# Performance work log

Measured on AMD Instinct MI355X. Metric: run time of the kernel, lower is better.

Reference implementation:

```python
import jax, jax.numpy as jnp
import numpy as np

N, E = 100000, 1600000
ENT, OCU, SAI, IJ = 64, 64, 64, 8


def setup_inputs() -> dict:
    key = jax.random.key(0)
    ks = jax.random.split(key, 14)

    def lin(k, fan_in, fan_out):
        s = 1.0 / np.sqrt(fan_in)
        kw, kb = jax.random.split(k)
        w = jax.random.uniform(kw, (fan_in, fan_out), minval=-s, maxval=s, dtype=jnp.float32)
        b = jax.random.uniform(kb, (fan_out,), minval=-s, maxval=s, dtype=jnp.float32)
        return w, b

    we_w1, we_b1 = lin(ks[0], 2 * ENT + 1 + IJ, OCU)
    we_w2, we_b2 = lin(ks[1], OCU, OCU)
    wx_w1, wx_b1 = lin(ks[2], OCU, OCU)
    wx_w2, wx_b2 = lin(ks[3], OCU, 1)
    wh_w1, wh_b1 = lin(ks[4], ENT + OCU, OCU)
    wh_w2, wh_b2 = lin(ks[5], OCU, SAI)
    wv_w1, wv_b1 = lin(ks[6], ENT, OCU)
    wv_w2, wv_b2 = lin(ks[7], OCU, 1)

    return {
        "h": jax.random.normal(ks[8], (N, ENT), dtype=jnp.float32),
        "x": jax.random.normal(ks[9], (N, 3), dtype=jnp.float32),
        "velocidade": jax.random.normal(ks[10], (N, 3), dtype=jnp.float32),
        "atributos_arestas": jax.random.normal(ks[11], (E, IJ), dtype=jnp.float32),
        "we_w1": we_w1, "we_b1": we_b1, "we_w2": we_w2, "we_b2": we_b2,
        "wx_w1": wx_w1, "wx_b1": wx_b1, "wx_w2": wx_w2, "wx_b2": wx_b2,
        "wh_w1": wh_w1, "wh_b1": wh_b1, "wh_w2": wh_w2, "wh_b2": wh_b2,
        "wv_w1": wv_w1, "wv_b1": wv_b1, "wv_w2": wv_w2, "wv_b2": wv_b2,
        "arestas": jax.random.randint(ks[12], (2, E), 0, N, dtype=jnp.int32),
    }


def reference(h, x, velocidade, atributos_arestas,
              we_w1, we_b1, we_w2, we_b2,
              wx_w1, wx_b1, wx_w2, wx_b2,
              wh_w1, wh_b1, wh_w2, wh_b2,
              wv_w1, wv_b1, wv_w2, wv_b2,
              arestas):
    linhas, cols = arestas[0], arestas[1]
    n = h.shape[0]

    # gather endpoint coordinates, radial distance per edge
    diferenca = x[linhas] - x[cols]                            # [E, 3]
    dif_radial = jnp.sum(diferenca * diferenca, axis=1, keepdims=True)  # [E, 1]

    # edge MLP phi_e on [h_i, h_j, ||x_i-x_j||^2, edge_attr]
    atributos = jnp.concatenate([h[linhas], h[cols], dif_radial, atributos_arestas], axis=1)
    m_ij = jnp.tanh(jnp.tanh(atributos @ we_w1 + we_b1) @ we_w2 + we_b2)   # [E, OCU]

    # phi_x: per-edge scalar gate on coordinate differences
    phi_x = jnp.tanh(jnp.tanh(m_ij @ wx_w1 + wx_b1) @ wx_w2 + wx_b2)       # [E, 1]

    # phi_v: per-node scalar gate on velocity
    phi_v = jnp.tanh(h @ wv_w1 + wv_b1) @ wv_w2 + wv_b2                    # [N, 1]

    # segment-mean of (diferenca * phi_x) over source nodes
    trans = diferenca * phi_x                                              # [E, 3]
    agg_sum = jax.ops.segment_sum(trans, linhas, num_segments=n)           # [N, 3]
    cnt = jax.ops.segment_sum(jnp.ones((E, 1), trans.dtype), linhas, num_segments=n)
    agg_mean = agg_sum / jnp.maximum(cnt, 1.0)

    velocidade_nova = velocidade * phi_v + agg_mean
    x_nova = x + velocidade_nova

    # segment-sum of edge messages, node update phi_h
    m_i = jax.ops.segment_sum(m_ij, linhas, num_segments=n)                # [N, OCU]
    h_cat = jnp.concatenate([h, m_i], axis=1)
    h_nova = jnp.tanh(h_cat @ wh_w1 + wh_b1) @ wh_w2 + wh_b2               # [N, SAI]

    return (h_nova, x_nova, velocidade_nova)
```

## Files before the change

### kernel.cpp

```cpp
#include <hip/hip_runtime.h>


typedef unsigned int uint;
typedef unsigned short u16;
typedef __attribute__((ext_vector_type(8))) short short8;
typedef __attribute__((ext_vector_type(4))) float f32x4;

#define UB_LO(u) __uint_as_float((u) << 16)
#define UB_HI(u) __uint_as_float((u) & 0xffff0000u)

__device__ __forceinline__ float fast_tanh(float x) {
    float e = __expf(2.0f * x);
    return 1.0f - 2.0f * __builtin_amdgcn_rcpf(e + 1.0f);
}
__device__ __forceinline__ u16 bf16rne(float f) {
    uint u = __float_as_uint(f);
    return (u16)((u + 0x7fffu + ((u >> 16) & 1u)) >> 16);
}
__device__ __forceinline__ uint packbf(float a, float b) {
    return (uint)bf16rne(a) | ((uint)bf16rne(b) << 16);
}
__device__ __forceinline__ uint packbf_fast(float a, float b) {
    return __builtin_amdgcn_perm(__float_as_uint(b), __float_as_uint(a), 0x07060302u);
}
__device__ __forceinline__ u16 trunc16(float f) {
    return (u16)(__float_as_uint(f) >> 16);
}
__device__ __forceinline__ int swzb(int b) { return b ^ ((b >> 3) & 0x70); }

__global__ void wprep_kernel(const float* __restrict__ we_w1, const float* __restrict__ we_w2,
                             const float* __restrict__ wx_w1, const float* __restrict__ wv_w1,
                             const float* __restrict__ wh_w1, const float* __restrict__ wh_w2,
                             u16* __restrict__ we1t, u16* __restrict__ we2t,
                             u16* __restrict__ wx1t, u16* __restrict__ wv1t,
                             u16* __restrict__ wh1t, u16* __restrict__ wh2t,
                             u16* __restrict__ wert) {
    int t = blockIdx.x * 256 + threadIdx.x;
    if (t < 8192) {
        int j = t >> 7, k = t & 127;
        we1t[t] = bf16rne(we_w1[k * 64 + j]);
        wh1t[t] = bf16rne(wh_w1[k * 64 + j]);
    }
    if (t < 4096) {
        int n = t >> 6, k = t & 63;
        we2t[t] = bf16rne(we_w2[k * 64 + n]);
        wx1t[t] = bf16rne(wx_w1[k * 64 + n]);
        wv1t[t] = bf16rne(wv_w1[k * 64 + n]);
        wh2t[t] = bf16rne(wh_w2[k * 64 + n]);
    }
    if (t < 2048) {
        int n = t >> 5, k = t & 31;
        float v = 0.0f;
        if (k == 0) v = we_w1[128 * 64 + n];
        else if (k <= 8) v = we_w1[(128 + k) * 64 + n];
        wert[t] = bf16rne(v);
    }
}

__global__ __launch_bounds__(256, 2)
void pre_mfma_kernel(const float* __restrict__ h, const float* __restrict__ we_b1,
                     const u16* __restrict__ we1t,
                     u16* __restrict__ HrB, u16* __restrict__ HcB, int N)
{
    __shared__ u16 X1[4096];
    __shared__ u16 X2[4096];
    const int tid = threadIdx.x, lane = tid & 63, wv = tid >> 6;
    const int nb = blockIdx.x * 64;
    const int el = tid >> 2, jg = tid & 3;
    const int fn = lane & 15, fk8 = (lane >> 4) * 8;

    {
        uint pk[8];
        if (nb + el < N) {
            const float4* h4 = (const float4*)(h + (size_t)(nb + el) * 64 + jg * 16);
            #pragma unroll
            for (int q = 0; q < 4; q++) {
                float4 v = h4[q];
                pk[2*q]   = packbf_fast(v.x, v.y);
                pk[2*q+1] = packbf_fast(v.z, v.w);
            }
        } else {
            #pragma unroll
            for (int q = 0; q < 8; q++) pk[q] = 0;
        }
        const int b0 = swzb(el * 128 + jg * 32), b1 = swzb(el * 128 + jg * 32 + 16);
        *(uint4*)(&X1[b0 >> 1]) = make_uint4(pk[0], pk[1], pk[2], pk[3]);
        *(uint4*)(&X1[b1 >> 1]) = make_uint4(pk[4], pk[5], pk[6], pk[7]);
    }
    __syncthreads();

    const int mb = wv * 16;
    short8 a0, a1;
    {
        const int ba = swzb((mb + fn) * 128 + fk8 * 2);
        const int bb = swzb((mb + fn) * 128 + 64 + fk8 * 2);
        a0 = *(const short8*)(&X1[ba >> 1]);
        a1 = *(const short8*)(&X1[bb >> 1]);
    }
    #pragma unroll
    for (int n0 = 0; n0 < 4; n0++) {
        uint4 bw0 = *(const uint4*)(we1t + (n0*16 + fn) * 128 + fk8);
        uint4 bw1 = *(const uint4*)(we1t + (n0*16 + fn) * 128 + 32 + fk8);
        const float bias = we_b1[n0 * 16 + fn];
        f32x4 q = {bias, bias, bias, bias};
        q = __builtin_amdgcn_mfma_f32_16x16x32_bf16(a0, __builtin_bit_cast(short8, bw0), q, 0, 0, 0);
        q = __builtin_amdgcn_mfma_f32_16x16x32_bf16(a1, __builtin_bit_cast(short8, bw1), q, 0, 0, 0);
        #pragma unroll
        for (int r2 = 0; r2 < 4; r2++) {
            const int m = mb + (lane >> 4) * 4 + r2;
            X2[swzb(m * 128 + (n0*16 + fn) * 2) >> 1] = bf16rne(q[r2]);
        }
    }
    __syncthreads();
    if (nb + el < N) {
        const int b0 = swzb(el * 128 + jg * 32), b1 = swzb(el * 128 + jg * 32 + 16);
        uint4 v0 = *(const uint4*)(&X2[b0 >> 1]);
        uint4 v1 = *(const uint4*)(&X2[b1 >> 1]);
        u16* o = HrB + (size_t)(nb + el) * 64 + jg * 16;
        *(uint4*)o = v0; *(uint4*)(o + 8) = v1;
    }
    __syncthreads();
    #pragma unroll
    for (int n0 = 0; n0 < 4; n0++) {
        uint4 bw0 = *(const uint4*)(we1t + (n0*16 + fn) * 128 + 64 + fk8);
        uint4 bw1 = *(const uint4*)(we1t + (n0*16 + fn) * 128 + 96 + fk8);
        f32x4 q = {0.f, 0.f, 0.f, 0.f};
        q = __builtin_amdgcn_mfma_f32_16x16x32_bf16(a0, __builtin_bit_cast(short8, bw0), q, 0, 0, 0);
        q = __builtin_amdgcn_mfma_f32_16x16x32_bf16(a1, __builtin_bit_cast(short8, bw1), q, 0, 0, 0);
        #pragma unroll
        for (int r2 = 0; r2 < 4; r2++) {
            const int m = mb + (lane >> 4) * 4 + r2;
            X2[swzb(m * 128 + (n0*16 + fn) * 2) >> 1] = bf16rne(q[r2]);
        }
    }
    __syncthreads();
    if (nb + el < N) {
        const int b0 = swzb(el * 128 + jg * 32), b1 = swzb(el * 128 + jg * 32 + 16);
        uint4 v0 = *(const uint4*)(&X2[b0 >> 1]);
        uint4 v1 = *(const uint4*)(&X2[b1 >> 1]);
        u16* o = HcB + (size_t)(nb + el) * 64 + jg * 16;
        *(uint4*)o = v0; *(uint4*)(o + 8) = v1;
    }
}

__global__ __launch_bounds__(256, 8)
void edge_mfma_kernel(const float* __restrict__ x, const float* __restrict__ eattr,
                      const int* __restrict__ perm, const int2* __restrict__ rc,
                      const u16* __restrict__ HrB, const u16* __restrict__ HcB,
                      const u16* __restrict__ wert,
                      const u16* __restrict__ we2t, const float* __restrict__ we_b2,
                      const u16* __restrict__ wx1t, const float* __restrict__ wx_b1,
                      const float* __restrict__ wx_w2, const float* __restrict__ wx_b2,
                      float* __restrict__ miF, float* __restrict__ aggF,
                      float* __restrict__ cntF, int E)
{
    __shared__ u16 T[4096];
    __shared__ float dS[64][3];
    __shared__ float pxS[64];
    __shared__ float radS[64];
    __shared__ int rS[64];

    const int tid = threadIdx.x, lane = tid & 63, wv = tid >> 6;
    int bid = blockIdx.x;
    const int nwg = gridDim.x;
    if ((nwg & 7) == 0) bid = (bid & 7) * (nwg >> 3) + (bid >> 3);
    const int sb = bid * 64;
    const int fn = lane & 15, fk8 = (lane >> 4) * 8;
    const int el = tid >> 2, jg = tid & 3;
    const int s = sb + el;
    const int mb = wv * 16;

    {
        int r = -1, c = 0;
        if (s < E) { int2 p2 = rc[s]; r = p2.x; c = p2.y; }
        if (jg == 0) rS[el] = r;
        uint pk[8];
        if (s < E) {
            if (jg == 0) {
                const float d0 = x[(size_t)r*3+0] - x[(size_t)c*3+0];
                const float d1 = x[(size_t)r*3+1] - x[(size_t)c*3+1];
                const float d2 = x[(size_t)r*3+2] - x[(size_t)c*3+2];
                dS[el][0] = d0; dS[el][1] = d1; dS[el][2] = d2;
                radS[el] = d0*d0 + d1*d1 + d2*d2;
            }
            uint4 ra = *(const uint4*)(HrB + (size_t)r * 64 + jg * 16);
            uint4 rb = *(const uint4*)(HrB + (size_t)r * 64 + jg * 16 + 8);
            uint4 ca = *(const uint4*)(HcB + (size_t)c * 64 + jg * 16);
            uint4 cb = *(const uint4*)(HcB + (size_t)c * 64 + jg * 16 + 8);
            uint rw[8] = {ra.x, ra.y, ra.z, ra.w, rb.x, rb.y, rb.z, rb.w};
            uint cw[8] = {ca.x, ca.y, ca.z, ca.w, cb.x, cb.y, cb.z, cb.w};
            #pragma unroll
            for (int q = 0; q < 8; q++) {
                const float lo = UB_LO(rw[q]) + UB_LO(cw[q]);
                const float hi = UB_HI(rw[q]) + UB_HI(cw[q]);
                pk[q] = packbf_fast(lo, hi);
            }
        } else {
            #pragma unroll
            for (int q = 0; q < 8; q++) pk[q] = 0;
        }
        const int b0 = swzb(el * 128 + jg * 32), b1 = swzb(el * 128 + jg * 32 + 16);
        *(uint4*)(&T[b0 >> 1]) = make_uint4(pk[0], pk[1], pk[2], pk[3]);
        *(uint4*)(&T[b1 >> 1]) = make_uint4(pk[4], pk[5], pk[6], pk[7]);
    }
    __syncthreads();

    uint ae[4] = {0, 0, 0, 0};
    {
        const int kc = lane >> 4;
        const int s2 = sb + mb + fn;
        if (kc < 2 && s2 < E) {
            const int e2 = perm[s2];
            const float4* ea4 = (const float4*)(eattr + (size_t)e2 * 8);
            if (kc == 0) {
                float4 u0 = ea4[0], u1 = ea4[1];
                const float rad = radS[mb + fn];
                ae[0] = packbf_fast(rad,  u0.x);
                ae[1] = packbf_fast(u0.y, u0.z);
                ae[2] = packbf_fast(u0.w, u1.x);
                ae[3] = packbf_fast(u1.y, u1.z);
            } else {
                float4 u1 = ea4[1];
                ae[0] = packbf_fast(u1.w, 0.0f);
            }
        }
    }
    const short8 a_e = __builtin_bit_cast(short8, *(uint4*)ae);

    #pragma unroll
    for (int n0 = 0; n0 < 4; n0++) {
        uint4 bw = *(const uint4*)(wert + (n0*16 + fn) * 32 + fk8);
        f32x4 q = {0.f, 0.f, 0.f, 0.f};
        q = __builtin_amdgcn_mfma_f32_16x16x32_bf16(a_e, __builtin_bit_cast(short8, bw), q, 0, 0, 0);
        #pragma unroll
        for (int r2 = 0; r2 < 4; r2++) {
            const int idx = swzb((mb + (lane >> 4) * 4 + r2) * 128 + (n0*16 + fn) * 2) >> 1;
            const float pre = q[r2] + UB_LO((uint)T[idx]);
            T[idx] = trunc16(fast_tanh(pre));
        }
    }

    short8 a0, a1;
    {
        const int ba = swzb((mb + fn) * 128 + fk8 * 2);
        const int bb = swzb((mb + fn) * 128 + 64 + fk8 * 2);
        a0 = *(const short8*)(&T[ba >> 1]);
        a1 = *(const short8*)(&T[bb >> 1]);
    }
    #pragma unroll
    for (int n0 = 0; n0 < 4; n0++) {
        uint4 bw0 = *(const uint4*)(we2t + (n0*16 + fn) * 64 + fk8);
        uint4 bw1 = *(const uint4*)(we2t + (n0*16 + fn) * 64 + 32 + fk8);
        const float bias = we_b2[n0 * 16 + fn];
        f32x4 q = {bias, bias, bias, bias};
        q = __builtin_amdgcn_mfma_f32_16x16x32_bf16(a0, __builtin_bit_cast(short8, bw0), q, 0, 0, 0);
        q = __builtin_amdgcn_mfma_f32_16x16x32_bf16(a1, __builtin_bit_cast(short8, bw1), q, 0, 0, 0);
        #pragma unroll
        for (int r2 = 0; r2 < 4; r2++) {
            const int m = mb + (lane >> 4) * 4 + r2;
            T[swzb(m * 128 + (n0*16 + fn) * 2) >> 1] = bf16rne(fast_tanh(q[r2]));
        }
    }

    short8 c0, c1;
    {
        const int ba = swzb((mb + fn) * 128 + fk8 * 2);
        const int bb = swzb((mb + fn) * 128 + 64 + fk8 * 2);
        c0 = *(const short8*)(&T[ba >> 1]);
        c1 = *(const short8*)(&T[bb >> 1]);
    }
    float pxp[4] = {0.f, 0.f, 0.f, 0.f};
    #pragma unroll
    for (int n0 = 0; n0 < 4; n0++) {
        uint4 bw0 = *(const uint4*)(wx1t + (n0*16 + fn) * 64 + fk8);
        uint4 bw1 = *(const uint4*)(wx1t + (n0*16 + fn) * 64 + 32 + fk8);
        const float bias = wx_b1[n0 * 16 + fn];
        f32x4 q = {bias, bias, bias, bias};
        q = __builtin_amdgcn_mfma_f32_16x16x32_bf16(c0, __builtin_bit_cast(short8, bw0), q, 0, 0, 0);
        q = __builtin_amdgcn_mfma_f32_16x16x32_bf16(c1, __builtin_bit_cast(short8, bw1), q, 0, 0, 0);
        const float wqn = wx_w2[n0 * 16 + fn];
        #pragma unroll
        for (int r2 = 0; r2 < 4; r2++) pxp[r2] += fast_tanh(q[r2]) * wqn;
    }
    #pragma unroll
    for (int off = 1; off < 16; off <<= 1) {
        #pragma unroll
        for (int r2 = 0; r2 < 4; r2++) pxp[r2] += __shfl_xor(pxp[r2], off, 64);
    }
    if (fn == 0) {
        const float bx2 = wx_b2[0];
        #pragma unroll
        for (int r2 = 0; r2 < 4; r2++) {
            const int m = mb + (lane >> 4) * 4 + r2;
            pxS[m] = fast_tanh(pxp[r2] + bx2);
        }
    }
    __syncthreads();

    const int w16 = wv * 16;
    for (int s0 = w16; s0 < w16 + 16; s0++) {
        const int r0 = rS[s0];
        if (r0 < 0) continue;
        if (s0 > 0 && rS[s0 - 1] == r0) continue;
        int s1 = s0 + 1;
        while (s1 < 64 && rS[s1] == r0) s1++;
        float msum = 0.0f, tsum = 0.0f;
        for (int t = s0; t < s1; t++) {
            msum += UB_LO((uint)T[swzb(t * 128 + lane * 2) >> 1]);
            if (lane < 3) tsum += dS[t][lane] * pxS[t];
        }
        atomicAdd(&miF[(size_t)r0 * 64 + lane], msum);
        if (lane < 3) atomicAdd(&aggF[(size_t)r0 * 3 + lane], tsum);
        if (lane == 3) atomicAdd(&cntF[r0], (float)(s1 - s0));
    }
}

__global__ __launch_bounds__(256, 2)
void aggnode_kernel(const float* __restrict__ h, const float* __restrict__ x,
                    const float* __restrict__ vel,
                    const float* __restrict__ miF, const float* __restrict__ aggF,
                    const float* __restrict__ cntF,
                    const u16* __restrict__ wv1t, const float* __restrict__ wv_b1,
                    const float* __restrict__ wv_w2, const float* __restrict__ wv_b2,
                    const u16* __restrict__ wh1t, const float* __restrict__ wh_b1,
                    const u16* __restrict__ wh2t, const float* __restrict__ wh_b2,
                    float* __restrict__ out_h, float* __restrict__ out_x,
                    float* __restrict__ out_v, int N)
{
    __shared__ u16 Xh[4096];
    __shared__ u16 Xm[4096];
    __shared__ float aggM[64][3];
    __shared__ float pvS[64];

    const int tid = threadIdx.x, lane = tid & 63, wv = tid >> 6;
    const int nb = blockIdx.x * 64;
    const int el = tid >> 2, jg = tid & 3;
    const int fn = lane & 15, fk8 = (lane >> 4) * 8;

    {
        uint pk[8];
        if (nb + el < N) {
            const float4* h4 = (const float4*)(h + (size_t)(nb + el) * 64 + jg * 16);
            #pragma unroll
            for (int q = 0; q < 4; q++) {
                float4 v = h4[q];
                pk[2*q]   = packbf_fast(v.x, v.y);
                pk[2*q+1] = packbf_fast(v.z, v.w);
            }
        } else {
            #pragma unroll
            for (int q = 0; q < 8; q++) pk[q] = 0;
        }
        const int b0 = swzb(el * 128 + jg * 32), b1 = swzb(el * 128 + jg * 32 + 16);
        *(uint4*)(&Xh[b0 >> 1]) = make_uint4(pk[0], pk[1], pk[2], pk[3]);
        *(uint4*)(&Xh[b1 >> 1]) = make_uint4(pk[4], pk[5], pk[6], pk[7]);
    }

    for (int t = 0; t < 16; t++) {
        const int ln = wv * 16 + t;
        const int n = nb + ln;
        float val = 0.0f;
        if (n < N) val = miF[(size_t)n * 64 + lane];
        Xm[swzb(ln * 128 + lane * 2) >> 1] = bf16rne(val);
        if (lane < 3 && n < N) {
            const float cf = cntF[n];
            aggM[ln][lane] = aggF[(size_t)n * 3 + lane] / fmaxf(cf, 1.0f);
        }
    }
    __syncthreads();

    const int mb = wv * 16;
    short8 a0, a1, b0, b1;
    {
        const int ba = swzb((mb + fn) * 128 + fk8 * 2);
        const int bb = swzb((mb + fn) * 128 + 64 + fk8 * 2);
        a0 = *(const short8*)(&Xh[ba >> 1]);
        a1 = *(const short8*)(&Xh[bb >> 1]);
        b0 = *(const short8*)(&Xm[ba >> 1]);
        b1 = *(const short8*)(&Xm[bb >> 1]);
    }

    float pvp[4] = {0.f, 0.f, 0.f, 0.f};
    #pragma unroll
    for (int n0 = 0; n0 < 4; n0++) {
        uint4 bw0 = *(const uint4*)(wv1t + (n0*16 + fn) * 64 + fk8);
        uint4 bw1 = *(const uint4*)(wv1t + (n0*16 + fn) * 64 + 32 + fk8);
        const float bias = wv_b1[n0 * 16 + fn];
        f32x4 q = {bias, bias, bias, bias};
        q = __builtin_amdgcn_mfma_f32_16x16x32_bf16(a0, __builtin_bit_cast(short8, bw0), q, 0, 0, 0);
        q = __builtin_amdgcn_mfma_f32_16x16x32_bf16(a1, __builtin_bit_cast(short8, bw1), q, 0, 0, 0);
        const float wqn = wv_w2[n0 * 16 + fn];
        #pragma unroll
        for (int r2 = 0; r2 < 4; r2++) pvp[r2] += fast_tanh(q[r2]) * wqn;
    }
    #pragma unroll
    for (int off = 1; off < 16; off <<= 1) {
        #pragma unroll
        for (int r2 = 0; r2 < 4; r2++) pvp[r2] += __shfl_xor(pvp[r2], off, 64);
    }
    if (fn == 0) {
        const float bv2 = wv_b2[0];
        #pragma unroll
        for (int r2 = 0; r2 < 4; r2++) pvS[mb + (lane >> 4) * 4 + r2] = pvp[r2] + bv2;
    }
    __syncthreads();

    #pragma unroll
    for (int n0 = 0; n0 < 4; n0++) {
        const u16* base = wh1t + (n0*16 + fn) * 128;
        uint4 bw0 = *(const uint4*)(base + fk8);
        uint4 bw1 = *(const uint4*)(base + 32 + fk8);
        uint4 bw2 = *(const uint4*)(base + 64 + fk8);
        uint4 bw3 = *(const uint4*)(base + 96 + fk8);
        const float bias = wh_b1[n0 * 16 + fn];
        f32x4 q = {bias, bias, bias, bias};
        q = __builtin_amdgcn_mfma_f32_16x16x32_bf16(a0, __builtin_bit_cast(short8, bw0), q, 0, 0, 0);
        q = __builtin_amdgcn_mfma_f32_16x16x32_bf16(a1, __builtin_bit_cast(short8, bw1), q, 0, 0, 0);
        q = __builtin_amdgcn_mfma_f32_16x16x32_bf16(b0, __builtin_bit_cast(short8, bw2), q, 0, 0, 0);
        q = __builtin_amdgcn_mfma_f32_16x16x32_bf16(b1, __builtin_bit_cast(short8, bw3), q, 0, 0, 0);
        #pragma unroll
        for (int r2 = 0; r2 < 4; r2++) {
            const int m = mb + (lane >> 4) * 4 + r2;
            Xm[swzb(m * 128 + (n0*16 + fn) * 2) >> 1] = bf16rne(fast_tanh(q[r2]));
        }
    }
    __syncthreads();

    short8 c0, c1;
    {
        const int ba = swzb((mb + fn) * 128 + fk8 * 2);
        const int bb = swzb((mb + fn) * 128 + 64 + fk8 * 2);
        c0 = *(const short8*)(&Xm[ba >> 1]);
        c1 = *(const short8*)(&Xm[bb >> 1]);
    }
    #pragma unroll
    for (int n0 = 0; n0 < 4; n0++) {
        uint4 bw0 = *(const uint4*)(wh2t + (n0*16 + fn) * 64 + fk8);
        uint4 bw1 = *(const uint4*)(wh2t + (n0*16 + fn) * 64 + 32 + fk8);
        const float bias = wh_b2[n0 * 16 + fn];
        f32x4 q = {bias, bias, bias, bias};
        q = __builtin_amdgcn_mfma_f32_16x16x32_bf16(c0, __builtin_bit_cast(short8, bw0), q, 0, 0, 0);
        q = __builtin_amdgcn_mfma_f32_16x16x32_bf16(c1, __builtin_bit_cast(short8, bw1), q, 0, 0, 0);
        #pragma unroll
        for (int r2 = 0; r2 < 4; r2++) {
            const int m = mb + (lane >> 4) * 4 + r2;
            if (nb + m < N) out_h[(size_t)(nb + m) * 64 + n0 * 16 + fn] = q[r2];
        }
    }

    if (tid < 64 && nb + tid < N) {
        const int n = nb + tid;
        const float pv = pvS[tid];
        #pragma unroll
        for (int d = 0; d < 3; d++) {
            const float am = aggM[tid][d];
            const float vn = vel[(size_t)n * 3 + d] * pv + am;
            out_v[(size_t)n * 3 + d] = vn;
            out_x[(size_t)n * 3 + d] = x[(size_t)n * 3 + d] + vn;
        }
    }
}

__global__ void hist_kernel(const int* __restrict__ rows, int* __restrict__ hist, int E) {
    int e = blockIdx.x * blockDim.x + threadIdx.x;
    if (e < E) atomicAdd(&hist[rows[e]], 1);
}

__global__ __launch_bounds__(256)
void scan1_kernel(const int* __restrict__ hist, int* __restrict__ bsum, int N) {
    const int t = threadIdx.x, b = blockIdx.x;
    const int base = b * 1024 + t * 4;
    int s = 0;
    #pragma unroll
    for (int q = 0; q < 4; q++) s += (base + q < N) ? hist[base + q] : 0;
    #pragma unroll
    for (int off = 1; off < 64; off <<= 1) s += __shfl_xor(s, off, 64);
    __shared__ int ws[4];
    if ((t & 63) == 0) ws[t >> 6] = s;
    __syncthreads();
    if (t == 0) bsum[b] = ws[0] + ws[1] + ws[2] + ws[3];
}

__global__ __launch_bounds__(256)
void scan2_kernel(int* __restrict__ bsum, int nb) {
    __shared__ int buf[1024];
    const int t = threadIdx.x;
    for (int i = t; i < nb; i += 256) buf[i] = bsum[i];
    __syncthreads();
    if (t == 0) {
        int run = 0;
        for (int i = 0; i < nb; i++) { int v = buf[i]; buf[i] = run; run += v; }
    }
    __syncthreads();
    for (int i = t; i < nb; i += 256) bsum[i] = buf[i];
}

__global__ __launch_bounds__(256)
void scan3_kernel(const int* __restrict__ hist, const int* __restrict__ bbase,
                  int* __restrict__ offs, int* __restrict__ cursor, int N) {
    const int t = threadIdx.x, b = blockIdx.x;
    const int base = b * 1024 + t * 4;
    int v[4];
    #pragma unroll
    for (int q = 0; q < 4; q++) v[q] = (base + q < N) ? hist[base + q] : 0;
    const int s = v[0] + v[1] + v[2] + v[3];
    const int lane = t & 63, wid = t >> 6;
    int inc = s;
    #pragma unroll
    for (int off = 1; off < 64; off <<= 1) {
        int u = __shfl_up(inc, off, 64);
        if (lane >= off) inc += u;
    }
    __shared__ int wtot[4];
    if (lane == 63) wtot[wid] = inc;
    __syncthreads();
    int wbase = 0;
    #pragma unroll
    for (int wq = 0; wq < 3; wq++) if (wq < wid) wbase += wtot[wq];
    int run = bbase[b] + wbase + (inc - s);
    #pragma unroll
    for (int q = 0; q < 4; q++) {
        const int i = base + q;
        if (i < N) { cursor[i] = run; run += v[q]; offs[i + 1] = run; }
    }
    if (b == 0 && t == 0) offs[0] = 0;
}

__global__ void scatter_kernel(const int* __restrict__ rows, const int* __restrict__ cols,
                               int* __restrict__ cursor,
                               int* __restrict__ perm, int2* __restrict__ rc, int E) {
    int e = blockIdx.x * blockDim.x + threadIdx.x;
    if (e < E) {
        int r = rows[e];
        int p = atomicAdd(&cursor[r], 1);
        perm[p] = e;
        rc[p] = make_int2(r, cols[e]);
    }
}

template<int BLK>
__global__ __launch_bounds__(BLK)
void edge_atomic_kernel(const float* __restrict__ h, const float* __restrict__ x,
                 const float* __restrict__ eattr,
                 const int* __restrict__ rows, const int* __restrict__ cols,
                 const float* __restrict__ we_w1, const float* __restrict__ we_b1,
                 const float* __restrict__ we_w2, const float* __restrict__ we_b2,
                 const float* __restrict__ wx_w1, const float* __restrict__ wx_b1,
                 const float* __restrict__ wx_w2, const float* __restrict__ wx_b2,
                 float* __restrict__ agg, float* __restrict__ cnt, float* __restrict__ mi,
                 int E)
{
    __shared__ float act[64][BLK];
    const int tid = threadIdx.x;
    const int e = blockIdx.x * BLK + tid;
    if (e >= E) return;

    const int r = rows[e];
    const int c = cols[e];
    const float d0 = x[(size_t)r*3+0] - x[(size_t)c*3+0];
    const float d1 = x[(size_t)r*3+1] - x[(size_t)c*3+1];
    const float d2 = x[(size_t)r*3+2] - x[(size_t)c*3+2];
    const float rad = d0*d0 + d1*d1 + d2*d2;

    float A[64];
    #pragma unroll
    for (int j = 0; j < 64; j++) A[j] = we_b1[j];
    const float* hr = h + (size_t)r * 64;
    const float* hc = h + (size_t)c * 64;
    #pragma unroll 4
    for (int k = 0; k < 64; k++) {
        const float a0 = hr[k];
        const float a1 = hc[k];
        const float* w0 = we_w1 + k * 64;
        const float* w1 = we_w1 + (64 + k) * 64;
        #pragma unroll
        for (int j = 0; j < 64; j++) A[j] += a0 * w0[j] + a1 * w1[j];
    }
    {
        const float* w = we_w1 + 128 * 64;
        #pragma unroll
        for (int j = 0; j < 64; j++) A[j] += rad * w[j];
    }
    const float* ea = eattr + (size_t)e * 8;
    #pragma unroll
    for (int k = 0; k < 8; k++) {
        const float a = ea[k];
        const float* w = we_w1 + (129 + k) * 64;
        #pragma unroll
        for (int j = 0; j < 64; j++) A[j] += a * w[j];
    }
    #pragma unroll
    for (int j = 0; j < 64; j++) act[j][tid] = fast_tanh(A[j]);

    float B[64];
    #pragma unroll
    for (int j = 0; j < 64; j++) B[j] = we_b2[j];
    #pragma unroll 4
    for (int k = 0; k < 64; k++) {
        const float a = act[k][tid];
        const float* w = we_w2 + k * 64;
        #pragma unroll
        for (int j = 0; j < 64; j++) B[j] += a * w[j];
    }
    #pragma unroll
    for (int j = 0; j < 64; j++) act[j][tid] = fast_tanh(B[j]);

    #pragma unroll
    for (int j = 0; j < 64; j++) A[j] = wx_b1[j];
    #pragma unroll 4
    for (int k = 0; k < 64; k++) {
        const float a = act[k][tid];
        const float* w = wx_w1 + k * 64;
        #pragma unroll
        for (int j = 0; j < 64; j++) A[j] += a * w[j];
    }
    float px = wx_b2[0];
    #pragma unroll
    for (int j = 0; j < 64; j++) px += fast_tanh(A[j]) * wx_w2[j];
    px = fast_tanh(px);

    atomicAdd(&agg[(size_t)r*3+0], d0 * px);
    atomicAdd(&agg[(size_t)r*3+1], d1 * px);
    atomicAdd(&agg[(size_t)r*3+2], d2 * px);
    atomicAdd(&cnt[r], 1.0f);
    float* mir = mi + (size_t)r * 64;
    #pragma unroll
    for (int j = 0; j < 64; j++) atomicAdd(&mir[j], act[j][tid]);
}

template<int BLK>
__global__ __launch_bounds__(BLK, 2)
void node_fb_kernel(const float* __restrict__ h, const float* __restrict__ x,
                 const float* __restrict__ vel,
                 const float* __restrict__ wh_w1, const float* __restrict__ wh_b1,
                 const float* __restrict__ wh_w2, const float* __restrict__ wh_b2,
                 const float* __restrict__ wv_w1, const float* __restrict__ wv_b1,
                 const float* __restrict__ wv_w2, const float* __restrict__ wv_b2,
                 const float* __restrict__ agg, const float* __restrict__ cnt,
                 const float* __restrict__ mi,
                 float* __restrict__ out_h, float* __restrict__ out_x, float* __restrict__ out_v,
                 int N)
{
    const int n = blockIdx.x * BLK + threadIdx.x;
    if (n >= N) return;

    const float* hn = h + (size_t)n * 64;
    const float* mn = mi + (size_t)n * 64;

    float A[64];
    #pragma unroll
    for (int j = 0; j < 64; j++) A[j] = wv_b1[j];
    #pragma unroll
    for (int k = 0; k < 64; k++) {
        const float a = hn[k];
        const float* w = wv_w1 + k * 64;
        #pragma unroll
        for (int j = 0; j < 64; j++) A[j] += a * w[j];
    }
    float pv = wv_b2[0];
    #pragma unroll
    for (int j = 0; j < 64; j++) pv += fast_tanh(A[j]) * wv_w2[j];

    #pragma unroll
    for (int j = 0; j < 64; j++) A[j] = wh_b1[j];
    #pragma unroll
    for (int k = 0; k < 64; k++) {
        const float a0 = hn[k];
        const float a1 = mn[k];
        const float* w0 = wh_w1 + k * 64;
        const float* w1 = wh_w1 + (64 + k) * 64;
        #pragma unroll
        for (int j = 0; j < 64; j++) A[j] += a0 * w0[j] + a1 * w1[j];
    }
    #pragma unroll
    for (int j = 0; j < 64; j++) A[j] = fast_tanh(A[j]);

    float B[64];
    #pragma unroll
    for (int j = 0; j < 64; j++) B[j] = wh_b2[j];
    #pragma unroll
    for (int k = 0; k < 64; k++) {
        const float a = A[k];
        const float* w = wh_w2 + k * 64;
        #pragma unroll
        for (int j = 0; j < 64; j++) B[j] += a * w[j];
    }
    float* oh = out_h + (size_t)n * 64;
    #pragma unroll
    for (int j = 0; j < 64; j++) oh[j] = B[j];

    const float inv = 1.0f / fmaxf(cnt[n], 1.0f);
    #pragma unroll
    for (int d = 0; d < 3; d++) {
        const float am = agg[(size_t)n*3 + d] * inv;
        const float vn = vel[(size_t)n*3 + d] * pv + am;
        out_v[(size_t)n*3 + d] = vn;
        out_x[(size_t)n*3 + d] = x[(size_t)n*3 + d] + vn;
    }
}

extern "C" void kernel_launch(void* const* d_in, const int* in_sizes, int n_in,
                              void* d_out, int out_size, void* d_ws, size_t ws_size,
                              hipStream_t stream) {
    const float* h      = (const float*)d_in[0];
    const float* x      = (const float*)d_in[1];
    const float* vel    = (const float*)d_in[2];
    const float* eattr  = (const float*)d_in[3];
    const float* we_w1  = (const float*)d_in[4];
    const float* we_b1  = (const float*)d_in[5];
    const float* we_w2  = (const float*)d_in[6];
    const float* we_b2  = (const float*)d_in[7];
    const float* wx_w1  = (const float*)d_in[8];
    const float* wx_b1  = (const float*)d_in[9];
    const float* wx_w2  = (const float*)d_in[10];
    const float* wx_b2  = (const float*)d_in[11];
    const float* wh_w1  = (const float*)d_in[12];
    const float* wh_b1  = (const float*)d_in[13];
    const float* wh_w2  = (const float*)d_in[14];
    const float* wh_b2  = (const float*)d_in[15];
    const float* wv_w1  = (const float*)d_in[16];
    const float* wv_b1  = (const float*)d_in[17];
    const float* wv_w2  = (const float*)d_in[18];
    const float* wv_b2  = (const float*)d_in[19];
    const int*   ar     = (const int*)d_in[20];

    const int N = in_sizes[0] / 64;
    const int E = in_sizes[20] / 2;
    const int* rows = ar;
    const int* cols = ar + E;

    float* out_h = (float*)d_out;
    float* out_x = out_h + (size_t)N * 64;
    float* out_v = out_x + (size_t)N * 3;

    u16* HrB = (u16*)d_out;
    u16* HcB = HrB + (size_t)N * 64;

    const int nbScan = (N + 1023) / 1024;

    char* p = (char*)d_ws;
    float* miF  = (float*)p; p += (size_t)N * 64 * sizeof(float);
    float* aggF = (float*)p; p += (size_t)N * 3 * sizeof(float);
    float* cntF = (float*)p; p += (size_t)N * sizeof(float);
    int*  hist  = (int*)p;   p += (size_t)N * sizeof(int);
    const size_t zero_bytes = (size_t)(p - (char*)d_ws);
    int*  offs  = (int*)p;   p += (size_t)(N + 1) * sizeof(int);
    int*  cursor= (int*)p;   p += (size_t)N * sizeof(int);
    int*  bsum  = (int*)p;   p += (size_t)(nbScan > 0 ? nbScan : 1) * sizeof(int);
    int*  perm  = (int*)p;   p += (size_t)E * sizeof(int);
    p = (char*)(((uintptr_t)p + 7) & ~(uintptr_t)7);
    int2* rc    = (int2*)p;  p += (size_t)E * sizeof(int2);
    p = (char*)(((uintptr_t)p + 63) & ~(uintptr_t)63);
    u16*  we1t = (u16*)p;   p += 64 * 128 * sizeof(u16);
    u16*  we2t = (u16*)p;   p += 64 * 64 * sizeof(u16);
    u16*  wx1t = (u16*)p;   p += 64 * 64 * sizeof(u16);
    u16*  wv1t = (u16*)p;   p += 64 * 64 * sizeof(u16);
    u16*  wh1t = (u16*)p;   p += 64 * 128 * sizeof(u16);
    u16*  wh2t = (u16*)p;   p += 64 * 64 * sizeof(u16);
    u16*  wert = (u16*)p;   p += 64 * 32 * sizeof(u16);
    const size_t needed = (size_t)(p - (char*)d_ws);

    if (ws_size >= needed && nbScan <= 1024) {
        hipMemsetAsync(d_ws, 0, zero_bytes, stream);
        hist_kernel<<<(E + 255) / 256, 256, 0, stream>>>(rows, hist, E);
        scan1_kernel<<<nbScan, 256, 0, stream>>>(hist, bsum, N);
        scan2_kernel<<<1, 256, 0, stream>>>(bsum, nbScan);
        scan3_kernel<<<nbScan, 256, 0, stream>>>(hist, bsum, offs, cursor, N);
        scatter_kernel<<<(E + 255) / 256, 256, 0, stream>>>(rows, cols, cursor, perm, rc, E);

        wprep_kernel<<<32, 256, 0, stream>>>(we_w1, we_w2, wx_w1, wv_w1, wh_w1, wh_w2,
                                             we1t, we2t, wx1t, wv1t, wh1t, wh2t, wert);
        pre_mfma_kernel<<<(N + 63) / 64, 256, 0, stream>>>(h, we_b1, we1t, HrB, HcB, N);

        edge_mfma_kernel<<<(E + 63) / 64, 256, 0, stream>>>(
            x, eattr, perm, rc, HrB, HcB,
            wert, we2t, we_b2, wx1t, wx_b1, wx_w2, wx_b2,
            miF, aggF, cntF, E);

        aggnode_kernel<<<(N + 63) / 64, 256, 0, stream>>>(
            h, x, vel, miF, aggF, cntF,
            wv1t, wv_b1, wv_w2, wv_b2,
            wh1t, wh_b1, wh2t, wh_b2,
            out_h, out_x, out_v, N);
    } else {
        float* agg2 = (float*)d_ws;
        float* cnt2 = agg2 + (size_t)N * 3;
        float* mi2  = cnt2 + N;
        hipMemsetAsync(d_ws, 0, (size_t)N * 68 * sizeof(float), stream);

        edge_atomic_kernel<128><<<(E + 127) / 128, 128, 0, stream>>>(
            h, x, eattr, rows, cols,
            we_w1, we_b1, we_w2, we_b2,
            wx_w1, wx_b1, wx_w2, wx_b2,
            agg2, cnt2, mi2, E);

        node_fb_kernel<128><<<(N + 127) / 128, 128, 0, stream>>>(
            h, x, vel,
            wh_w1, wh_b1, wh_w2, wh_b2,
            wv_w1, wv_b1, wv_w2, wv_b2,
            agg2, cnt2, mi2, out_h, out_x, out_v, N);
    }
}
```

Baseline: 552.0 us.

## Pack sorted edge records with bf16 attributes, merge wprep/hist, single-kernel scan

Measured after the change: 720.8 us. 1.31x slower.

```diff
diff --git a/kernel.cpp b/kernel.cpp
--- a/kernel.cpp
+++ b/kernel.cpp
@@ -28,32 +28,39 @@
 }
 __device__ __forceinline__ int swzb(int b) { return b ^ ((b >> 3) & 0x70); }
 
-__global__ void wprep_kernel(const float* __restrict__ we_w1, const float* __restrict__ we_w2,
-                             const float* __restrict__ wx_w1, const float* __restrict__ wv_w1,
-                             const float* __restrict__ wh_w1, const float* __restrict__ wh_w2,
-                             u16* __restrict__ we1t, u16* __restrict__ we2t,
-                             u16* __restrict__ wx1t, u16* __restrict__ wv1t,
-                             u16* __restrict__ wh1t, u16* __restrict__ wh2t,
-                             u16* __restrict__ wert) {
-    int t = blockIdx.x * 256 + threadIdx.x;
-    if (t < 8192) {
-        int j = t >> 7, k = t & 127;
-        we1t[t] = bf16rne(we_w1[k * 64 + j]);
-        wh1t[t] = bf16rne(wh_w1[k * 64 + j]);
-    }
-    if (t < 4096) {
-        int n = t >> 6, k = t & 63;
-        we2t[t] = bf16rne(we_w2[k * 64 + n]);
-        wx1t[t] = bf16rne(wx_w1[k * 64 + n]);
-        wv1t[t] = bf16rne(wv_w1[k * 64 + n]);
-        wh2t[t] = bf16rne(wh_w2[k * 64 + n]);
-    }
-    if (t < 2048) {
-        int n = t >> 5, k = t & 31;
-        float v = 0.0f;
-        if (k == 0) v = we_w1[128 * 64 + n];
-        else if (k <= 8) v = we_w1[(128 + k) * 64 + n];
-        wert[t] = bf16rne(v);
+__global__ void wprep_hist_kernel(const float* __restrict__ we_w1, const float* __restrict__ we_w2,
+                                  const float* __restrict__ wx_w1, const float* __restrict__ wv_w1,
+                                  const float* __restrict__ wh_w1, const float* __restrict__ wh_w2,
+                                  u16* __restrict__ we1t, u16* __restrict__ we2t,
+                                  u16* __restrict__ wx1t, u16* __restrict__ wv1t,
+                                  u16* __restrict__ wh1t, u16* __restrict__ wh2t,
+                                  u16* __restrict__ wert,
+                                  const int* __restrict__ rows, int* __restrict__ hist, int E) {
+    const int b = blockIdx.x;
+    if (b < 32) {
+        int t = b * 256 + threadIdx.x;
+        if (t < 8192) {
+            int j = t >> 7, k = t & 127;
+            we1t[t] = bf16rne(we_w1[k * 64 + j]);
+            wh1t[t] = bf16rne(wh_w1[k * 64 + j]);
+        }
+        if (t < 4096) {
+            int n = t >> 6, k = t & 63;
+            we2t[t] = bf16rne(we_w2[k * 64 + n]);
+            wx1t[t] = bf16rne(wx_w1[k * 64 + n]);
+            wv1t[t] = bf16rne(wv_w1[k * 64 + n]);
+            wh2t[t] = bf16rne(wh_w2[k * 64 + n]);
+        }
+        if (t < 2048) {
+            int n = t >> 5, k = t & 31;
+            float v = 0.0f;
+            if (k == 0) v = we_w1[128 * 64 + n];
+            else if (k <= 8) v = we_w1[(128 + k) * 64 + n];
+            wert[t] = bf16rne(v);
+        }
+    } else {
+        int e = (b - 32) * 256 + threadIdx.x;
+        if (e < E) atomicAdd(&hist[rows[e]], 1);
     }
 }
 
@@ -144,8 +151,8 @@
 }
 
 __global__ __launch_bounds__(256, 8)
-void edge_mfma_kernel(const float* __restrict__ x, const float* __restrict__ eattr,
-                      const int* __restrict__ perm, const int2* __restrict__ rc,
+void edge_mfma_kernel(const float* __restrict__ x,
+                      const uint* __restrict__ rec,
                       const u16* __restrict__ HrB, const u16* __restrict__ HcB,
                       const u16* __restrict__ wert,
                       const u16* __restrict__ we2t, const float* __restrict__ we_b2,
@@ -172,7 +179,7 @@
 
     {
         int r = -1, c = 0;
-        if (s < E) { int2 p2 = rc[s]; r = p2.x; c = p2.y; }
+        if (s < E) { int2 p2 = *(const int2*)(rec + (size_t)s * 8); r = p2.x; c = p2.y; }
         if (jg == 0) rS[el] = r;
         uint pk[8];
         if (s < E) {
@@ -210,18 +217,15 @@
         const int kc = lane >> 4;
         const int s2 = sb + mb + fn;
         if (kc < 2 && s2 < E) {
-            const int e2 = perm[s2];
-            const float4* ea4 = (const float4*)(eattr + (size_t)e2 * 8);
+            const uint4 ue = *(const uint4*)(rec + (size_t)s2 * 8 + 4);
             if (kc == 0) {
-                float4 u0 = ea4[0], u1 = ea4[1];
                 const float rad = radS[mb + fn];
-                ae[0] = packbf_fast(rad,  u0.x);
-                ae[1] = packbf_fast(u0.y, u0.z);
-                ae[2] = packbf_fast(u0.w, u1.x);
-                ae[3] = packbf_fast(u1.y, u1.z);
+                ae[0] = __builtin_amdgcn_perm(ue.x, __float_as_uint(rad), 0x05040302u);
+                ae[1] = __builtin_amdgcn_alignbit(ue.y, ue.x, 16);
+                ae[2] = __builtin_amdgcn_alignbit(ue.z, ue.y, 16);
+                ae[3] = __builtin_amdgcn_alignbit(ue.w, ue.z, 16);
             } else {
-                float4 u1 = ea4[1];
-                ae[0] = packbf_fast(u1.w, 0.0f);
+                ae[0] = ue.w >> 16;
             }
         }
     }
@@ -461,80 +465,60 @@
     }
 }
 
-__global__ void hist_kernel(const int* __restrict__ rows, int* __restrict__ hist, int E) {
-    int e = blockIdx.x * blockDim.x + threadIdx.x;
-    if (e < E) atomicAdd(&hist[rows[e]], 1);
-}
-
-__global__ __launch_bounds__(256)
-void scan1_kernel(const int* __restrict__ hist, int* __restrict__ bsum, int N) {
-    const int t = threadIdx.x, b = blockIdx.x;
-    const int base = b * 1024 + t * 4;
+__global__ __launch_bounds__(1024)
+void scan_kernel(const int* __restrict__ hist, int* __restrict__ offs,
+                 int* __restrict__ cursor, int N) {
+    const int tid = threadIdx.x;
+    const int chunk = (N + 1023) / 1024;
+    const int beg = tid * chunk;
+    const int end = (beg + chunk < N) ? beg + chunk : N;
+
     int s = 0;
-    #pragma unroll
-    for (int q = 0; q < 4; q++) s += (base + q < N) ? hist[base + q] : 0;
-    #pragma unroll
-    for (int off = 1; off < 64; off <<= 1) s += __shfl_xor(s, off, 64);
-    __shared__ int ws[4];
-    if ((t & 63) == 0) ws[t >> 6] = s;
-    __syncthreads();
-    if (t == 0) bsum[b] = ws[0] + ws[1] + ws[2] + ws[3];
-}
-
-__global__ __launch_bounds__(256)
-void scan2_kernel(int* __restrict__ bsum, int nb) {
-    __shared__ int buf[1024];
-    const int t = threadIdx.x;
-    for (int i = t; i < nb; i += 256) buf[i] = bsum[i];
-    __syncthreads();
-    if (t == 0) {
-        int run = 0;
-        for (int i = 0; i < nb; i++) { int v = buf[i]; buf[i] = run; run += v; }
-    }
-    __syncthreads();
-    for (int i = t; i < nb; i += 256) bsum[i] = buf[i];
-}
-
-__global__ __launch_bounds__(256)
-void scan3_kernel(const int* __restrict__ hist, const int* __restrict__ bbase,
-                  int* __restrict__ offs, int* __restrict__ cursor, int N) {
-    const int t = threadIdx.x, b = blockIdx.x;
-    const int base = b * 1024 + t * 4;
-    int v[4];
-    #pragma unroll
-    for (int q = 0; q < 4; q++) v[q] = (base + q < N) ? hist[base + q] : 0;
-    const int s = v[0] + v[1] + v[2] + v[3];
-    const int lane = t & 63, wid = t >> 6;
+    for (int i = beg; i < end; i++) s += hist[i];
+
+    __shared__ int wsum[16];
+    const int lane = tid & 63, wid = tid >> 6;
     int inc = s;
     #pragma unroll
     for (int off = 1; off < 64; off <<= 1) {
-        int u = __shfl_up(inc, off, 64);
-        if (lane >= off) inc += u;
-    }
-    __shared__ int wtot[4];
-    if (lane == 63) wtot[wid] = inc;
-    __syncthreads();
-    int wbase = 0;
-    #pragma unroll
-    for (int wq = 0; wq < 3; wq++) if (wq < wid) wbase += wtot[wq];
-    int run = bbase[b] + wbase + (inc - s);
-    #pragma unroll
-    for (int q = 0; q < 4; q++) {
-        const int i = base + q;
-        if (i < N) { cursor[i] = run; run += v[q]; offs[i + 1] = run; }
-    }
-    if (b == 0 && t == 0) offs[0] = 0;
+        int t = __shfl_up(inc, off, 64);
+        if (lane >= off) inc += t;
+    }
+    if (lane == 63) wsum[wid] = inc;
+    __syncthreads();
+    if (wid == 0 && lane < 16) {
+        int v = wsum[lane];
+        #pragma unroll
+        for (int off = 1; off < 16; off <<= 1) {
+            int t = __shfl_up(v, off, 64);
+            if (lane >= off) v += t;
+        }
+        wsum[lane] = v;
+    }
+    __syncthreads();
+    const int wbase = (wid > 0) ? wsum[wid - 1] : 0;
+    int run = wbase + inc - s;
+    for (int i = beg; i < end; i++) {
+        cursor[i] = run;
+        run += hist[i];
+        offs[i + 1] = run;
+    }
+    if (tid == 0) offs[0] = 0;
 }
 
 __global__ void scatter_kernel(const int* __restrict__ rows, const int* __restrict__ cols,
-                               int* __restrict__ cursor,
-                               int* __restrict__ perm, int2* __restrict__ rc, int E) {
+                               const float* __restrict__ eattr,
+                               int* __restrict__ cursor, uint* __restrict__ rec, int E) {
     int e = blockIdx.x * blockDim.x + threadIdx.x;
     if (e < E) {
         int r = rows[e];
         int p = atomicAdd(&cursor[r], 1);
-        perm[p] = e;
-        rc[p] = make_int2(r, cols[e]);
+        const float4* ea4 = (const float4*)(eattr + (size_t)e * 8);
+        float4 u0 = ea4[0], u1 = ea4[1];
+        *(int2*)(rec + (size_t)p * 8) = make_int2(r, cols[e]);
+        *(uint4*)(rec + (size_t)p * 8 + 4) =
+            make_uint4(packbf(u0.x, u0.y), packbf(u0.z, u0.w),
+                       packbf(u1.x, u1.y), packbf(u1.z, u1.w));
     }
 }
 
@@ -736,8 +720,6 @@
     u16* HrB = (u16*)d_out;
     u16* HcB = HrB + (size_t)N * 64;
 
-    const int nbScan = (N + 1023) / 1024;
-
     char* p = (char*)d_ws;
     float* miF  = (float*)p; p += (size_t)N * 64 * sizeof(float);
     float* aggF = (float*)p; p += (size_t)N * 3 * sizeof(float);
@@ -746,10 +728,8 @@
     const size_t zero_bytes = (size_t)(p - (char*)d_ws);
     int*  offs  = (int*)p;   p += (size_t)(N + 1) * sizeof(int);
     int*  cursor= (int*)p;   p += (size_t)N * sizeof(int);
-    int*  bsum  = (int*)p;   p += (size_t)(nbScan > 0 ? nbScan : 1) * sizeof(int);
-    int*  perm  = (int*)p;   p += (size_t)E * sizeof(int);
-    p = (char*)(((uintptr_t)p + 7) & ~(uintptr_t)7);
-    int2* rc    = (int2*)p;  p += (size_t)E * sizeof(int2);
+    p = (char*)(((uintptr_t)p + 31) & ~(uintptr_t)31);
+    uint* rec   = (uint*)p;  p += (size_t)E * 8 * sizeof(uint);
     p = (char*)(((uintptr_t)p + 63) & ~(uintptr_t)63);
     u16*  we1t = (u16*)p;   p += 64 * 128 * sizeof(u16);
     u16*  we2t = (u16*)p;   p += 64 * 64 * sizeof(u16);
@@ -760,20 +740,18 @@
     u16*  wert = (u16*)p;   p += 64 * 32 * sizeof(u16);
     const size_t needed = (size_t)(p - (char*)d_ws);
 
-    if (ws_size >= needed && nbScan <= 1024) {
+    if (ws_size >= needed) {
         hipMemsetAsync(d_ws, 0, zero_bytes, stream);
-        hist_kernel<<<(E + 255) / 256, 256, 0, stream>>>(rows, hist, E);
-        scan1_kernel<<<nbScan, 256, 0, stream>>>(hist, bsum, N);
-        scan2_kernel<<<1, 256, 0, stream>>>(bsum, nbScan);
-        scan3_kernel<<<nbScan, 256, 0, stream>>>(hist, bsum, offs, cursor, N);
-        scatter_kernel<<<(E + 255) / 256, 256, 0, stream>>>(rows, cols, cursor, perm, rc, E);
-
-        wprep_kernel<<<32, 256, 0, stream>>>(we_w1, we_w2, wx_w1, wv_w1, wh_w1, wh_w2,
-                                             we1t, we2t, wx1t, wv1t, wh1t, wh2t, wert);
+        wprep_hist_kernel<<<32 + (E + 255) / 256, 256, 0, stream>>>(
+            we_w1, we_w2, wx_w1, wv_w1, wh_w1, wh_w2,
+            we1t, we2t, wx1t, wv1t, wh1t, wh2t, wert, rows, hist, E);
+        scan_kernel<<<1, 1024, 0, stream>>>(hist, offs, cursor, N);
+        scatter_kernel<<<(E + 255) / 256, 256, 0, stream>>>(rows, cols, eattr, cursor, rec, E);
+
         pre_mfma_kernel<<<(N + 63) / 64, 256, 0, stream>>>(h, we_b1, we1t, HrB, HcB, N);
 
         edge_mfma_kernel<<<(E + 63) / 64, 256, 0, stream>>>(
-            x, eattr, perm, rc, HrB, HcB,
+            x, rec, HrB, HcB,
             wert, we2t, we_b2, wx1t, wx_b1, wx_w2, wx_b2,
             miF, aggF, cntF, E);
 
```
